# Kernel optimization log

Hardware: AMD Instinct MI355X
Metric: run time of the kernel (lower is better)

The kernel has to match this reference:

```python
import jax, jax.numpy as jnp
import numpy as np

N, E, T, F, HID, NCLS = 50000, 800000, 6, 64, 48, 2
LN_EPS = 1e-5


def setup_inputs() -> dict:
    key = jax.random.key(0)
    ks = jax.random.split(key, 24)
    p = lambda k, shape, s=0.1: jax.random.normal(k, shape, dtype=jnp.float32) * s
    inp = {
        "x_seq": jax.random.normal(ks[0], (T, N, F), dtype=jnp.float32),
        "edge_index": jax.random.randint(ks[1], (2, E), 0, N, dtype=jnp.int64),
        "edge_weight": jax.random.uniform(ks[2], (E,), dtype=jnp.float32),
        # GCN layer 0
        "W0": p(ks[3], (F, HID)), "b0": jnp.zeros((HID,), jnp.float32),
        "g0": jnp.ones((HID,), jnp.float32), "be0": jnp.zeros((HID,), jnp.float32),
        # GCN layer 1
        "W1": p(ks[4], (HID, HID)), "b1": jnp.zeros((HID,), jnp.float32),
        "g1": jnp.ones((HID,), jnp.float32), "be1": jnp.zeros((HID,), jnp.float32),
        # GRU (torch gate order: r, z, n)
        "W_ih": p(ks[5], (3 * HID, HID)), "W_hh": p(ks[6], (3 * HID, HID)),
        "b_ih": jnp.zeros((3 * HID,), jnp.float32), "b_hh": jnp.zeros((3 * HID,), jnp.float32),
        # classifier MLP
        "Wc1": p(ks[7], (HID, HID // 2)), "bc1": jnp.zeros((HID // 2,), jnp.float32),
        "Wc2": p(ks[8], (HID // 2, NCLS)), "bc2": jnp.zeros((NCLS,), jnp.float32),
    }
    return inp


def _layer_norm(x, g, b):
    mu = x.mean(-1, keepdims=True)
    var = ((x - mu) ** 2).mean(-1, keepdims=True)
    return (x - mu) * jax.lax.rsqrt(var + LN_EPS) * g + b


def reference(x_seq, edge_index, edge_weight, W0, b0, g0, be0, W1, b1, g1, be1,
              W_ih, W_hh, b_ih, b_hh, Wc1, bc1, Wc2, bc2):
    n = x_seq.shape[1]
    hid = W0.shape[1]
    row, col = edge_index[0], edge_index[1]
    # PyG GCNConv default: add self-loops (weight 1), symmetric normalization
    loop = jnp.arange(n)
    row_f = jnp.concatenate([row, loop])
    col_f = jnp.concatenate([col, loop])
    w_f = jnp.concatenate([edge_weight, jnp.ones((n,), edge_weight.dtype)])
    deg = jax.ops.segment_sum(w_f, col_f, num_segments=n)
    dis = jnp.where(deg > 0, jax.lax.rsqrt(jnp.maximum(deg, 1e-12)), 0.0)
    norm = dis[row_f] * w_f * dis[col_f]  # [E+N]

    def gcn(x, W, b):
        h = x @ W                              # [N, hid]
        msg = h[row_f] * norm[:, None]         # [E+N, hid]
        return jax.ops.segment_sum(msg, col_f, num_segments=n) + b

    def spatial(x_t):
        # layer 0: no residual (in_dim != hid)
        h1 = jax.nn.relu(_layer_norm(gcn(x_t, W0, b0), g0, be0))
        # layer 1: residual (dropout is eval-mode no-op)
        h2 = jax.nn.relu(_layer_norm(gcn(h1, W1, b1), g1, be1)) + h1
        return h2

    # sequential map over T keeps per-step [E,hid] message buffers small
    H = jax.lax.map(spatial, x_seq)            # [T, N, hid]

    def gru_step(h, x_t):
        gi = x_t @ W_ih.T + b_ih               # [N, 3*hid]
        gh = h @ W_hh.T + b_hh
        i_r, i_z, i_n = jnp.split(gi, 3, axis=-1)
        h_r, h_z, h_n = jnp.split(gh, 3, axis=-1)
        r = jax.nn.sigmoid(i_r + h_r)
        z = jax.nn.sigmoid(i_z + h_z)
        nv = jnp.tanh(i_n + r * h_n)
        h_new = (1.0 - z) * nv + z * h
        return h_new, None

    h0 = jnp.zeros((n, hid), x_seq.dtype)
    z_last, _ = jax.lax.scan(gru_step, h0, H)  # last hidden state [N, hid]

    logits = jax.nn.relu(z_last @ Wc1 + bc1) @ Wc2 + bc2  # [N, 2]
    return logits
```

## Files before the change

### kernel.cpp

```cpp
#include <hip/hip_runtime.h>
#include <math.h>

#define NN 50000
#define NE 800000
#define TT 6
#define HID 48
#define NB 196
#define LR 65

__device__ __forceinline__ float sigmoidf_(float x){ return 1.0f/(1.0f+__expf(-x)); }
__device__ __forceinline__ float tanhf_(float x){
  float xc = fminf(fmaxf(x,-15.f),15.f);
  float t = __expf(2.f*xc);
  return (t-1.f)/(t+1.f);
}
__device__ __forceinline__ unsigned f2bf(float x){
  unsigned u = __float_as_uint(x);
  return (u + 0x7fffu + ((u>>16)&1u)) >> 16;
}
__device__ __forceinline__ unsigned pack2(float a, float b){
  return f2bf(a) | (f2bf(b)<<16);
}
__device__ __forceinline__ float bflo(unsigned u){ return __uint_as_float(u<<16); }
__device__ __forceinline__ float bfhi(unsigned u){ return __uint_as_float(u & 0xffff0000u); }

struct U3 { unsigned x,y,z; };

__device__ __forceinline__ int block_scan_incl(int x, int* wsum){
  int lane = threadIdx.x & 63, w = threadIdx.x >> 6;
  int v = x;
#pragma unroll
  for(int d=1; d<64; d<<=1){
    int u = __shfl_up(v, d, 64);
    if(lane >= d) v += u;
  }
  if(lane==63) wsum[w] = v;
  __syncthreads();
  int add = 0;
#pragma unroll
  for(int k=0;k<3;k++) if(w>k) add += wsum[k];
  return v + add;
}

__global__ __launch_bounds__(256) void k_setup(int* cnt,
                                               const float* __restrict__ Wih, const float* __restrict__ Whh,
                                               float* Wg){
  int i = blockIdx.x*256+threadIdx.x;
  if(i<NN) cnt[i]=0;
  if(i < 6*48*48){
    int w = i/2304, rem = i%2304;
    int k = rem/48, g8 = rem%48;
    int g = g8>>3, j = g8&7;
    int col = w*8+j;
    float v = (g<3) ? Wih[(g*48+col)*48 + k] : Whh[((g-3)*48+col)*48 + k];
    Wg[i] = v;
  }
}

__global__ __launch_bounds__(256) void k_cnt(const int* __restrict__ ei, int* cnt, int* pos){
  int e = blockIdx.x*256+threadIdx.x;
  if(e<NE){
    int c = ei[NE+e];
    pos[e] = atomicAdd(&cnt[c], 1);
  }
}

__global__ __launch_bounds__(256) void k_partA(const int* __restrict__ cnt, int* bsum){
  __shared__ int wsum[4];
  int i = blockIdx.x*256+threadIdx.x;
  int x = (i<NN)? cnt[i] : 0;
  int lane = threadIdx.x & 63, w = threadIdx.x >> 6;
  int v = x;
#pragma unroll
  for(int m=32;m>=1;m>>=1) v += __shfl_xor(v, m, 64);
  if(lane==0) wsum[w]=v;
  __syncthreads();
  if(threadIdx.x==0) bsum[blockIdx.x] = wsum[0]+wsum[1]+wsum[2]+wsum[3];
}

__global__ __launch_bounds__(256) void k_midB(const int* __restrict__ bsum, int* bpre, int* offs){
  __shared__ int wsum[4];
  int t = threadIdx.x;
  int x = (t<NB)? bsum[t] : 0;
  int incl = block_scan_incl(x, wsum);
  if(t<NB) bpre[t] = incl - x;
  if(t==255) offs[NN] = incl;
}

__global__ __launch_bounds__(256) void k_offsC(const int* __restrict__ cnt, const int* __restrict__ bpre,
                                               int* offs){
  __shared__ int wsum[4];
  int i = blockIdx.x*256+threadIdx.x;
  int x = (i<NN)? cnt[i] : 0;
  int incl = block_scan_incl(x, wsum);
  if(i<NN) offs[i] = bpre[blockIdx.x] + incl - x;
}

__global__ __launch_bounds__(256) void k_scatter(const int* __restrict__ ei, const float* __restrict__ ew,
                                                 const int* __restrict__ offs, const int* __restrict__ pos,
                                                 int2* __restrict__ csr){
  int e = blockIdx.x*256+threadIdx.x;
  if(e<NE){
    int c = ei[NE+e];
    int2 v; v.x = ei[e]; v.y = __float_as_int(ew[e]);
    csr[offs[c]+pos[e]] = v;
  }
}

__global__ __launch_bounds__(256) void k_deg(const int2* __restrict__ csr, const int* __restrict__ offs,
                                             float* dis){
  int i = blockIdx.x*256+threadIdx.x;
  if(i<NN){
    float s = 1.f;
    int e0=offs[i], e1=offs[i+1];
    for(int j=e0;j<e1;j++) s += __int_as_float(csr[j].y);
    dis[i] = rsqrtf(s);
  }
}

__global__ __launch_bounds__(256) void k_normE(int2* __restrict__ csr, const float* __restrict__ dis){
  int j = blockIdx.x*256+threadIdx.x;
  if(j<NE){
    int2 v = csr[j];
    v.y = __float_as_int(dis[v.x]*__int_as_float(v.y));
    csr[j] = v;
  }
}

__global__ __launch_bounds__(256) void k_mm0(const float* __restrict__ X, const float* __restrict__ W,
                                             unsigned* __restrict__ A){
  int s = __builtin_amdgcn_readfirstlane(threadIdx.x>>6);
  int n = blockIdx.x*64 + (threadIdx.x&63);
  if(n>=NN) return;
  const float* xb = X + (long long)n*64;
  const float* wb = W + 12*s;
  float acc[TT][12];
#pragma unroll
  for(int t=0;t<TT;t++)
#pragma unroll
    for(int j=0;j<12;j++) acc[t][j]=0.f;
#pragma unroll 2
  for(int k4=0;k4<16;k4++){
    float4 xv[TT];
#pragma unroll
    for(int t=0;t<TT;t++) xv[t] = *reinterpret_cast<const float4*>(xb + (long long)t*NN*64 + 4*k4);
#pragma unroll
    for(int q=0;q<4;q++){
      const float* wr = wb + (4*k4+q)*HID;
      float w[12];
#pragma unroll
      for(int j=0;j<12;j++) w[j]=wr[j];
#pragma unroll
      for(int t=0;t<TT;t++){
        float xs = (&xv[t].x)[q];
#pragma unroll
        for(int j=0;j<12;j++) acc[t][j] = fmaf(xs, w[j], acc[t][j]);
      }
    }
  }
  unsigned buf[36];
#pragma unroll
  for(int j=0;j<12;j++){
    buf[3*j  ]=pack2(acc[0][j],acc[1][j]);
    buf[3*j+1]=pack2(acc[2][j],acc[3][j]);
    buf[3*j+2]=pack2(acc[4][j],acc[5][j]);
  }
  uint4* o4 = reinterpret_cast<uint4*>(A + (long long)n*144 + 36*s);
#pragma unroll
  for(int q=0;q<9;q++) o4[q] = make_uint4(buf[4*q],buf[4*q+1],buf[4*q+2],buf[4*q+3]);
}

__global__ __launch_bounds__(256) void k_mm1(const float* __restrict__ X, const float* __restrict__ W,
                                             unsigned* __restrict__ A){
  int s = __builtin_amdgcn_readfirstlane(threadIdx.x>>6);
  int n = blockIdx.x*64 + (threadIdx.x&63);
  if(n>=NN) return;
  const float* xb = X + (long long)n*(TT*HID);
  const float* wb = W + 12*s;
  float acc[TT][12];
#pragma unroll
  for(int t=0;t<TT;t++)
#pragma unroll
    for(int j=0;j<12;j++) acc[t][j]=0.f;
#pragma unroll 2
  for(int k4=0;k4<12;k4++){
    float4 xv[TT];
#pragma unroll
    for(int t=0;t<TT;t++) xv[t] = *reinterpret_cast<const float4*>(xb + t*HID + 4*k4);
#pragma unroll
    for(int q=0;q<4;q++){
      const float* wr = wb + (4*k4+q)*HID;
      float w[12];
#pragma unroll
      for(int j=0;j<12;j++) w[j]=wr[j];
#pragma unroll
      for(int t=0;t<TT;t++){
        float xs = (&xv[t].x)[q];
#pragma unroll
        for(int j=0;j<12;j++) acc[t][j] = fmaf(xs, w[j], acc[t][j]);
      }
    }
  }
  unsigned buf[36];
#pragma unroll
  for(int j=0;j<12;j++){
    buf[3*j  ]=pack2(acc[0][j],acc[1][j]);
    buf[3*j+1]=pack2(acc[2][j],acc[3][j]);
    buf[3*j+2]=pack2(acc[4][j],acc[5][j]);
  }
  uint4* o4 = reinterpret_cast<uint4*>(A + (long long)n*144 + 36*s);
#pragma unroll
  for(int q=0;q<9;q++) o4[q] = make_uint4(buf[4*q],buf[4*q+1],buf[4*q+2],buf[4*q+3]);
}

__global__ __launch_bounds__(256) void k_agg(const unsigned* __restrict__ A, const float* __restrict__ bias,
                                             const float* __restrict__ gain, const float* __restrict__ beta,
                                             const float* __restrict__ resid, float* __restrict__ out,
                                             const int* __restrict__ offs, const int2* __restrict__ csr,
                                             const float* __restrict__ dis){
  int wid = (blockIdx.x*256+threadIdx.x)>>6;
  int lane = threadIdx.x & 63;
  if(wid>=NN) return;
  const bool act = lane<HID;
  const int f = act? lane : (HID-1);
  float dn = dis[wid];
  float acc[TT];
  {
    U3 v = *reinterpret_cast<const U3*>(A + (long long)wid*144 + 3*f);
    acc[0]=dn*bflo(v.x); acc[1]=dn*bfhi(v.x);
    acc[2]=dn*bflo(v.y); acc[3]=dn*bfhi(v.y);
    acc[4]=dn*bflo(v.z); acc[5]=dn*bfhi(v.z);
  }
  int e0=offs[wid], e1=offs[wid+1];
  int e=e0;
  for(; e+3<e1; e+=4){
    int2 i0=csr[e], i1=csr[e+1], i2=csr[e+2], i3=csr[e+3];
    U3 d0 = *reinterpret_cast<const U3*>(A + (long long)i0.x*144 + 3*f);
    U3 d1 = *reinterpret_cast<const U3*>(A + (long long)i1.x*144 + 3*f);
    U3 d2 = *reinterpret_cast<const U3*>(A + (long long)i2.x*144 + 3*f);
    U3 d3 = *reinterpret_cast<const U3*>(A + (long long)i3.x*144 + 3*f);
    float n0=__int_as_float(i0.y), n1=__int_as_float(i1.y);
    float n2=__int_as_float(i2.y), n3=__int_as_float(i3.y);
    acc[0]=fmaf(n0,bflo(d0.x),acc[0]); acc[1]=fmaf(n0,bfhi(d0.x),acc[1]);
    acc[2]=fmaf(n0,bflo(d0.y),acc[2]); acc[3]=fmaf(n0,bfhi(d0.y),acc[3]);
    acc[4]=fmaf(n0,bflo(d0.z),acc[4]); acc[5]=fmaf(n0,bfhi(d0.z),acc[5]);
    acc[0]=fmaf(n1,bflo(d1.x),acc[0]); acc[1]=fmaf(n1,bfhi(d1.x),acc[1]);
    acc[2]=fmaf(n1,bflo(d1.y),acc[2]); acc[3]=fmaf(n1,bfhi(d1.y),acc[3]);
    acc[4]=fmaf(n1,bflo(d1.z),acc[4]); acc[5]=fmaf(n1,bfhi(d1.z),acc[5]);
    acc[0]=fmaf(n2,bflo(d2.x),acc[0]); acc[1]=fmaf(n2,bfhi(d2.x),acc[1]);
    acc[2]=fmaf(n2,bflo(d2.y),acc[2]); acc[3]=fmaf(n2,bfhi(d2.y),acc[3]);
    acc[4]=fmaf(n2,bflo(d2.z),acc[4]); acc[5]=fmaf(n2,bfhi(d2.z),acc[5]);
    acc[0]=fmaf(n3,bflo(d3.x),acc[0]); acc[1]=fmaf(n3,bfhi(d3.x),acc[1]);
    acc[2]=fmaf(n3,bflo(d3.y),acc[2]); acc[3]=fmaf(n3,bfhi(d3.y),acc[3]);
    acc[4]=fmaf(n3,bflo(d3.z),acc[4]); acc[5]=fmaf(n3,bfhi(d3.z),acc[5]);
  }
  for(; e<e1; ++e){
    int2 i0=csr[e];
    U3 d0 = *reinterpret_cast<const U3*>(A + (long long)i0.x*144 + 3*f);
    float n0=__int_as_float(i0.y);
    acc[0]=fmaf(n0,bflo(d0.x),acc[0]); acc[1]=fmaf(n0,bfhi(d0.x),acc[1]);
    acc[2]=fmaf(n0,bflo(d0.y),acc[2]); acc[3]=fmaf(n0,bfhi(d0.y),acc[3]);
    acc[4]=fmaf(n0,bflo(d0.z),acc[4]); acc[5]=fmaf(n0,bfhi(d0.z),acc[5]);
  }
  float bb = bias[f], gg = gain[f], be = beta[f];
  const float rn = 1.0f/HID;
#pragma unroll
  for(int t=0;t<TT;t++){
    float val = fmaf(acc[t], dn, bb);
    float v = act? val : 0.f;
    float s = v, s2 = v*v;
#pragma unroll
    for(int m=32;m>=1;m>>=1){
      s  += __shfl_xor(s,  m, 64);
      s2 += __shfl_xor(s2, m, 64);
    }
    float mu  = s*rn;
    float var = fmaxf(s2*rn - mu*mu, 0.f);
    float y = (val-mu)*rsqrtf(var+1e-5f)*gg + be;
    y = fmaxf(y, 0.f);
    long long oidx = (long long)wid*(TT*HID) + t*HID + f;
    if(resid) y += resid[oidx];
    if(act) out[oidx] = y;
  }
}

__global__ __launch_bounds__(384) void k_gruF(const float* __restrict__ X,
                                              const float* __restrict__ Wg,
                                              const float* __restrict__ bih, const float* __restrict__ bhh,
                                              const float* __restrict__ Wc1, const float* __restrict__ bc1,
                                              const float* __restrict__ Wc2, const float* __restrict__ bc2,
                                              float* __restrict__ out){
  __shared__ float xbuf[48*LR];
  __shared__ float hbuf[48*LR];
  int tid = threadIdx.x;
  int wv = __builtin_amdgcn_readfirstlane(tid>>6);
  int lane = tid & 63;
  int f0 = wv*8;
  long long nbase = (long long)blockIdx.x*64;

  for(int i=tid;i<48*LR;i+=384) hbuf[i]=0.f;

  float rb[8], zb[8], nbi[8], nbh[8];
#pragma unroll
  for(int j=0;j<8;j++){
    int f=f0+j;
    rb[j]  = bih[f]    + bhh[f];
    zb[j]  = bih[48+f] + bhh[48+f];
    nbi[j] = bih[96+f];
    nbh[j] = bhh[96+f];
  }

  for(int t=0;t<TT;t++){
#pragma unroll
    for(int i=0;i<2;i++){
      int c = tid + 384*i;
      int nd = c/12, fc = c - nd*12;
      long long gn = nbase + nd; if(gn>NN-1) gn=NN-1;
      float4 xv = *reinterpret_cast<const float4*>(X + gn*(TT*HID) + t*HID + fc*4);
      int base = (fc*4)*LR + nd;
      xbuf[base]      = xv.x;
      xbuf[base+LR]   = xv.y;
      xbuf[base+2*LR] = xv.z;
      xbuf[base+3*LR] = xv.w;
    }
    __syncthreads();

    float ra[8],za[8],ia[8],ha[8];
#pragma unroll
    for(int j=0;j<8;j++){ ra[j]=za[j]=ia[j]=ha[j]=0.f; }

#pragma unroll 2
    for(int k=0;k<48;k++){
      const float* wp = Wg + ((wv*48 + k)*48);
      float ws[48];
#pragma unroll
      for(int q=0;q<48;q++) ws[q]=wp[q];
      float xk = xbuf[k*LR+lane];
      float hk = hbuf[k*LR+lane];
#pragma unroll
      for(int j=0;j<8;j++){
        ra[j]=fmaf(xk,ws[j],   ra[j]); ra[j]=fmaf(hk,ws[24+j],ra[j]);
        za[j]=fmaf(xk,ws[8+j], za[j]); za[j]=fmaf(hk,ws[32+j],za[j]);
        ia[j]=fmaf(xk,ws[16+j],ia[j]); ha[j]=fmaf(hk,ws[40+j],ha[j]);
      }
    }

    float hn[8];
#pragma unroll
    for(int j=0;j<8;j++){
      float r  = sigmoidf_(ra[j]+rb[j]);
      float zg = sigmoidf_(za[j]+zb[j]);
      float ng = tanhf_(ia[j]+nbi[j] + r*(ha[j]+nbh[j]));
      hn[j] = (1.f-zg)*ng + zg*hbuf[(f0+j)*LR+lane];
    }
    __syncthreads();
#pragma unroll
    for(int j=0;j<8;j++) hbuf[(f0+j)*LR+lane] = hn[j];
  }
  __syncthreads();

  if(wv==0){
    long long gn = nbase + lane;
    if(gn<NN){
      float hv[24];
#pragma unroll
      for(int j=0;j<24;j++) hv[j]=bc1[j];
      for(int k=0;k<HID;k++){
        float xk = hbuf[k*LR+lane];
        const float* wr = Wc1 + k*24;
#pragma unroll
        for(int j=0;j<24;j++) hv[j] = fmaf(xk, wr[j], hv[j]);
      }
      float l0=bc2[0], l1=bc2[1];
#pragma unroll
      for(int j=0;j<24;j++){
        float a = fmaxf(hv[j],0.f);
        l0 = fmaf(a, Wc2[2*j],   l0);
        l1 = fmaf(a, Wc2[2*j+1], l1);
      }
      reinterpret_cast<float2*>(out)[gn] = make_float2(l0,l1);
    }
  }
}

static inline size_t al256(size_t x){ return (x+255)&~(size_t)255; }

extern "C" void kernel_launch(void* const* d_in, const int* in_sizes, int n_in,
                              void* d_out, int out_size, void* d_ws, size_t ws_size,
                              hipStream_t stream){
  const float* x_seq=(const float*)d_in[0];
  const int*   ei   =(const int*)d_in[1];
  const float* ew   =(const float*)d_in[2];
  const float* W0=(const float*)d_in[3];  const float* b0=(const float*)d_in[4];
  const float* g0=(const float*)d_in[5];  const float* be0=(const float*)d_in[6];
  const float* W1=(const float*)d_in[7];  const float* b1=(const float*)d_in[8];
  const float* g1=(const float*)d_in[9];  const float* be1=(const float*)d_in[10];
  const float* Wih=(const float*)d_in[11];const float* Whh=(const float*)d_in[12];
  const float* bih=(const float*)d_in[13];const float* bhh=(const float*)d_in[14];
  const float* Wc1=(const float*)d_in[15];const float* bc1=(const float*)d_in[16];
  const float* Wc2=(const float*)d_in[17];const float* bc2=(const float*)d_in[18];
  float* outp=(float*)d_out;

  char* p=(char*)d_ws; size_t off=0;
  auto alloc=[&](size_t bytes)->void*{ void* r=p+off; off=al256(off+bytes); return r; };
  float* dis    =(float*)alloc((size_t)NN*4);
  int*   cnt    =(int*)  alloc((size_t)NN*4);
  int*   offs   =(int*)  alloc((size_t)(NN+1)*4);
  int*   bsum   =(int*)  alloc((size_t)NB*4);
  int*   bpre   =(int*)  alloc((size_t)NB*4);
  int*   pos    =(int*)  alloc((size_t)NE*4);
  int2*  csr    =(int2*) alloc((size_t)NE*8);
  float* Wg     =(float*)alloc((size_t)6*48*48*4);
  unsigned* A   =(unsigned*)alloc((size_t)NN*576 + 1024);
  float* h1     =(float*)alloc((size_t)NN*TT*HID*4);
  float* h2     =(float*)alloc((size_t)NN*TT*HID*4);

  const int GN=(NN+255)/256, GE=(NE+255)/256;
  const int GMM=(NN+63)/64;
  const int GAGG=(NN*64+255)/256;
  const int GGRU=(NN+63)/64;

  k_setup  <<<GN,256,0,stream>>>(cnt,Wih,Whh,Wg);
  k_cnt    <<<GE,256,0,stream>>>(ei,cnt,pos);
  k_partA  <<<NB,256,0,stream>>>(cnt,bsum);
  k_midB   <<<1,256,0,stream>>>(bsum,bpre,offs);
  k_offsC  <<<NB,256,0,stream>>>(cnt,bpre,offs);
  k_scatter<<<GE,256,0,stream>>>(ei,ew,offs,pos,csr);
  k_deg    <<<GN,256,0,stream>>>(csr,offs,dis);
  k_normE  <<<GE,256,0,stream>>>(csr,dis);

  k_mm0<<<GMM,256,0,stream>>>(x_seq, W0, A);
  k_agg<<<GAGG,256,0,stream>>>(A,b0,g0,be0,nullptr,h1,offs,csr,dis);
  k_mm1<<<GMM,256,0,stream>>>(h1, W1, A);
  k_agg<<<GAGG,256,0,stream>>>(A,b1,g1,be1,h1,h2,offs,csr,dis);
  k_gruF<<<GGRU,384,0,stream>>>(h2, Wg, bih,bhh, Wc1,bc1,Wc2,bc2, outp);
}
```

Before: 702.9 us.

## Split GRU input projection into parallel fp16 precompute kernel, recurrence-only GRU

```diff
diff --git a/kernel.cpp b/kernel.cpp
--- a/kernel.cpp
+++ b/kernel.cpp
@@ -1,4 +1,5 @@
 #include <hip/hip_runtime.h>
+#include <hip/hip_fp16.h>
 #include <math.h>
 
 #define NN 50000
@@ -23,6 +24,12 @@
 }
 __device__ __forceinline__ float bflo(unsigned u){ return __uint_as_float(u<<16); }
 __device__ __forceinline__ float bfhi(unsigned u){ return __uint_as_float(u & 0xffff0000u); }
+__device__ __forceinline__ unsigned f2h(float x){
+  return (unsigned)__half_as_ushort(__float2half(x));
+}
+__device__ __forceinline__ float h2f(unsigned u){
+  return __half2float(__ushort_as_half((unsigned short)(u & 0xffffu)));
+}
 
 struct U3 { unsigned x,y,z; };
 
@@ -44,16 +51,19 @@
 
 __global__ __launch_bounds__(256) void k_setup(int* cnt,
                                                const float* __restrict__ Wih, const float* __restrict__ Whh,
-                                               float* Wg){
+                                               float* WxT, float* Whg){
   int i = blockIdx.x*256+threadIdx.x;
   if(i<NN) cnt[i]=0;
-  if(i < 6*48*48){
-    int w = i/2304, rem = i%2304;
-    int k = rem/48, g8 = rem%48;
-    int g = g8>>3, j = g8&7;
-    int col = w*8+j;
-    float v = (g<3) ? Wih[(g*48+col)*48 + k] : Whh[((g-3)*48+col)*48 + k];
-    Wg[i] = v;
+  if(i < 48*144){
+    int k = i/144, gf = i%144;
+    WxT[i] = Wih[gf*48 + k];
+  }
+  if(i < 6*48*24){
+    int wv = i/1152, r = i%1152;
+    int k = r/24, c = r%24;
+    int g = c>>3, j = c&7;
+    int gf = g*48 + wv*8 + j;
+    Whg[i] = Whh[gf*48 + k];
   }
 }
 
@@ -284,102 +294,135 @@
   }
 }
 
-__global__ __launch_bounds__(384) void k_gruF(const float* __restrict__ X,
-                                              const float* __restrict__ Wg,
-                                              const float* __restrict__ bih, const float* __restrict__ bhh,
+__global__ __launch_bounds__(384) void k_gi(const float* __restrict__ X,
+                                            const float* __restrict__ WxT,
+                                            const float* __restrict__ bih,
+                                            unsigned* __restrict__ gi){
+  int wv = __builtin_amdgcn_readfirstlane(threadIdx.x>>6);
+  int lane = threadIdx.x & 63;
+  long long n = (long long)blockIdx.x*64 + lane;
+  long long gn = (n < NN)? n : (NN-1);
+  const float* xb = X + gn*(TT*HID) + wv*HID;
+  const bool wr = (n < NN);
+#pragma unroll 1
+  for(int g2=0; g2<6; g2++){
+    float acc[24];
+#pragma unroll
+    for(int j=0;j<24;j++) acc[j] = bih[g2*24+j];
+#pragma unroll 2
+    for(int k4=0;k4<12;k4++){
+      float4 xv = *reinterpret_cast<const float4*>(xb + 4*k4);
+#pragma unroll
+      for(int q=0;q<4;q++){
+        const float* wp = WxT + (4*k4+q)*144 + g2*24;
+        float ws[24];
+#pragma unroll
+        for(int j=0;j<24;j++) ws[j]=wp[j];
+        float xs = (&xv.x)[q];
+#pragma unroll
+        for(int j=0;j<24;j++) acc[j]=fmaf(xs, ws[j], acc[j]);
+      }
+    }
+    if(wr){
+      unsigned* ob = gi + ((long long)(wv*72 + g2*12))*NN + n;
+#pragma unroll
+      for(int m=0;m<12;m++){
+        unsigned u = f2h(acc[2*m]) | (f2h(acc[2*m+1])<<16);
+        ob[(long long)m*NN] = u;
+      }
+    }
+  }
+}
+
+__global__ __launch_bounds__(384) void k_gruH(const unsigned* __restrict__ gi,
+                                              const float* __restrict__ Whg,
+                                              const float* __restrict__ bhh,
                                               const float* __restrict__ Wc1, const float* __restrict__ bc1,
                                               const float* __restrict__ Wc2, const float* __restrict__ bc2,
                                               float* __restrict__ out){
-  __shared__ float xbuf[48*LR];
-  __shared__ float hbuf[48*LR];
+  __shared__ float hbuf[2][48*LR];
   int tid = threadIdx.x;
   int wv = __builtin_amdgcn_readfirstlane(tid>>6);
   int lane = tid & 63;
   int f0 = wv*8;
-  long long nbase = (long long)blockIdx.x*64;
-
-  for(int i=tid;i<48*LR;i+=384) hbuf[i]=0.f;
-
-  float rb[8], zb[8], nbi[8], nbh[8];
+  long long n = (long long)blockIdx.x*64 + lane;
+  long long gn = (n<NN)? n : (NN-1);
+
+  for(int i=tid;i<48*LR;i+=384) hbuf[0][i]=0.f;
+
+  float rb[8], zb[8], nb[8], hprev[8];
 #pragma unroll
   for(int j=0;j<8;j++){
-    int f=f0+j;
-    rb[j]  = bih[f]    + bhh[f];
-    zb[j]  = bih[48+f] + bhh[48+f];
-    nbi[j] = bih[96+f];
-    nbh[j] = bhh[96+f];
-  }
-
+    rb[j]=bhh[f0+j]; zb[j]=bhh[48+f0+j]; nb[j]=bhh[96+f0+j];
+    hprev[j]=0.f;
+  }
+  __syncthreads();
+
+  int cur=0;
   for(int t=0;t<TT;t++){
-#pragma unroll
-    for(int i=0;i<2;i++){
-      int c = tid + 384*i;
-      int nd = c/12, fc = c - nd*12;
-      long long gn = nbase + nd; if(gn>NN-1) gn=NN-1;
-      float4 xv = *reinterpret_cast<const float4*>(X + gn*(TT*HID) + t*HID + fc*4);
-      int base = (fc*4)*LR + nd;
-      xbuf[base]      = xv.x;
-      xbuf[base+LR]   = xv.y;
-      xbuf[base+2*LR] = xv.z;
-      xbuf[base+3*LR] = xv.w;
+    const unsigned* gb = gi + (long long)t*72*NN + gn;
+    unsigned gpk[12];
+#pragma unroll
+    for(int m=0;m<4;m++){
+      gpk[m]   = gb[(long long)(      f0/2+m)*NN];
+      gpk[4+m] = gb[(long long)(24 +  f0/2+m)*NN];
+      gpk[8+m] = gb[(long long)(48 +  f0/2+m)*NN];
+    }
+    float ra[8], za[8], ha[8];
+#pragma unroll
+    for(int j=0;j<8;j++){ ra[j]=0.f; za[j]=0.f; ha[j]=0.f; }
+    const float* hb = &hbuf[cur][0];
+#pragma unroll 4
+    for(int k=0;k<48;k++){
+      const float* wp = Whg + (wv*48+k)*24;
+      float ws[24];
+#pragma unroll
+      for(int q=0;q<24;q++) ws[q]=wp[q];
+      float hk = hb[k*LR+lane];
+#pragma unroll
+      for(int j=0;j<8;j++){
+        ra[j]=fmaf(hk,ws[j],   ra[j]);
+        za[j]=fmaf(hk,ws[8+j], za[j]);
+        ha[j]=fmaf(hk,ws[16+j],ha[j]);
+      }
+    }
+    float* hw = &hbuf[cur^1][0];
+#pragma unroll
+    for(int j=0;j<8;j++){
+      unsigned pr=gpk[j>>1], pz=gpk[4+(j>>1)], pn=gpk[8+(j>>1)];
+      float gir = (j&1)? h2f(pr>>16) : h2f(pr);
+      float giz = (j&1)? h2f(pz>>16) : h2f(pz);
+      float gin = (j&1)? h2f(pn>>16) : h2f(pn);
+      float r  = sigmoidf_(ra[j]+rb[j]+gir);
+      float zg = sigmoidf_(za[j]+zb[j]+giz);
+      float ng = tanhf_(gin + r*(ha[j]+nb[j]));
+      float hv = (1.f-zg)*ng + zg*hprev[j];
+      hprev[j]=hv;
+      hw[(f0+j)*LR+lane]=hv;
     }
     __syncthreads();
-
-    float ra[8],za[8],ia[8],ha[8];
-#pragma unroll
-    for(int j=0;j<8;j++){ ra[j]=za[j]=ia[j]=ha[j]=0.f; }
-
-#pragma unroll 2
-    for(int k=0;k<48;k++){
-      const float* wp = Wg + ((wv*48 + k)*48);
-      float ws[48];
-#pragma unroll
-      for(int q=0;q<48;q++) ws[q]=wp[q];
-      float xk = xbuf[k*LR+lane];
-      float hk = hbuf[k*LR+lane];
-#pragma unroll
-      for(int j=0;j<8;j++){
-        ra[j]=fmaf(xk,ws[j],   ra[j]); ra[j]=fmaf(hk,ws[24+j],ra[j]);
-        za[j]=fmaf(xk,ws[8+j], za[j]); za[j]=fmaf(hk,ws[32+j],za[j]);
-        ia[j]=fmaf(xk,ws[16+j],ia[j]); ha[j]=fmaf(hk,ws[40+j],ha[j]);
-      }
-    }
-
-    float hn[8];
-#pragma unroll
-    for(int j=0;j<8;j++){
-      float r  = sigmoidf_(ra[j]+rb[j]);
-      float zg = sigmoidf_(za[j]+zb[j]);
-      float ng = tanhf_(ia[j]+nbi[j] + r*(ha[j]+nbh[j]));
-      hn[j] = (1.f-zg)*ng + zg*hbuf[(f0+j)*LR+lane];
-    }
-    __syncthreads();
-#pragma unroll
-    for(int j=0;j<8;j++) hbuf[(f0+j)*LR+lane] = hn[j];
-  }
-  __syncthreads();
-
-  if(wv==0){
-    long long gn = nbase + lane;
-    if(gn<NN){
-      float hv[24];
-#pragma unroll
-      for(int j=0;j<24;j++) hv[j]=bc1[j];
-      for(int k=0;k<HID;k++){
-        float xk = hbuf[k*LR+lane];
-        const float* wr = Wc1 + k*24;
-#pragma unroll
-        for(int j=0;j<24;j++) hv[j] = fmaf(xk, wr[j], hv[j]);
-      }
-      float l0=bc2[0], l1=bc2[1];
-#pragma unroll
-      for(int j=0;j<24;j++){
-        float a = fmaxf(hv[j],0.f);
-        l0 = fmaf(a, Wc2[2*j],   l0);
-        l1 = fmaf(a, Wc2[2*j+1], l1);
-      }
-      reinterpret_cast<float2*>(out)[gn] = make_float2(l0,l1);
-    }
+    cur^=1;
+  }
+
+  if(wv==0 && n<NN){
+    const float* hb=&hbuf[cur][0];
+    float hv[24];
+#pragma unroll
+    for(int j=0;j<24;j++) hv[j]=bc1[j];
+    for(int k=0;k<HID;k++){
+      float xk = hb[k*LR+lane];
+      const float* wr2 = Wc1 + k*24;
+#pragma unroll
+      for(int j=0;j<24;j++) hv[j] = fmaf(xk, wr2[j], hv[j]);
+    }
+    float l0=bc2[0], l1=bc2[1];
+#pragma unroll
+    for(int j=0;j<24;j++){
+      float a = fmaxf(hv[j],0.f);
+      l0 = fmaf(a, Wc2[2*j],   l0);
+      l1 = fmaf(a, Wc2[2*j+1], l1);
+    }
+    reinterpret_cast<float2*>(out)[n] = make_float2(l0,l1);
   }
 }
 
@@ -410,17 +453,19 @@
   int*   bpre   =(int*)  alloc((size_t)NB*4);
   int*   pos    =(int*)  alloc((size_t)NE*4);
   int2*  csr    =(int2*) alloc((size_t)NE*8);
-  float* Wg     =(float*)alloc((size_t)6*48*48*4);
+  float* WxT    =(float*)alloc((size_t)48*144*4);
+  float* Whg    =(float*)alloc((size_t)6*48*24*4);
   unsigned* A   =(unsigned*)alloc((size_t)NN*576 + 1024);
   float* h1     =(float*)alloc((size_t)NN*TT*HID*4);
   float* h2     =(float*)alloc((size_t)NN*TT*HID*4);
+  unsigned* gi  =(unsigned*)A;
 
   const int GN=(NN+255)/256, GE=(NE+255)/256;
   const int GMM=(NN+63)/64;
   const int GAGG=(NN*64+255)/256;
   const int GGRU=(NN+63)/64;
 
-  k_setup  <<<GN,256,0,stream>>>(cnt,Wih,Whh,Wg);
+  k_setup  <<<GN,256,0,stream>>>(cnt,Wih,Whh,WxT,Whg);
   k_cnt    <<<GE,256,0,stream>>>(ei,cnt,pos);
   k_partA  <<<NB,256,0,stream>>>(cnt,bsum);
   k_midB   <<<1,256,0,stream>>>(bsum,bpre,offs);
@@ -433,5 +478,6 @@
   k_agg<<<GAGG,256,0,stream>>>(A,b0,g0,be0,nullptr,h1,offs,csr,dis);
   k_mm1<<<GMM,256,0,stream>>>(h1, W1, A);
   k_agg<<<GAGG,256,0,stream>>>(A,b1,g1,be1,h1,h2,offs,csr,dis);
-  k_gruF<<<GGRU,384,0,stream>>>(h2, Wg, bih,bhh, Wc1,bc1,Wc2,bc2, outp);
-}
+  k_gi  <<<GMM,384,0,stream>>>(h2, WxT, bih, gi);
+  k_gruH<<<GGRU,384,0,stream>>>(gi, Whg, bhh, Wc1,bc1,Wc2,bc2, outp);
+}
```

After: 756.0 us. +7.6%, slower.
